# Performance work log

Hardware: AMD Instinct MI355X
Metric: run time of the kernel (lower is better)

## Reference

```python
import math
import jax, jax.numpy as jnp
import numpy as np

H = 4
C_HID = 32

def setup_inputs() -> dict:
    key = jax.random.key(0)
    ks = jax.random.split(key, 8)
    B, N, C = 1, 256, 128
    q_x = jax.random.normal(ks[0], (B, N, N, C), dtype=jnp.float32)
    kv_x = jax.random.normal(ks[1], (B, N, N, C), dtype=jnp.float32)
    tri_bias = jax.random.normal(ks[2], (B, 1, H, N, N), dtype=jnp.float32)
    mask_bias = jnp.zeros((B, N, 1, 1, N), dtype=jnp.float32)
    mask = jnp.ones((B, N, N, N), dtype=jnp.float32)
    s = 1.0 / math.sqrt(C)
    Wq = jax.random.normal(ks[3], (C, H * C_HID), dtype=jnp.float32) * s
    Wk = jax.random.normal(ks[4], (C, H * C_HID), dtype=jnp.float32) * s
    Wv = jax.random.normal(ks[5], (C, H * C_HID), dtype=jnp.float32) * s
    Wg = jax.random.normal(ks[6], (C, H * C_HID), dtype=jnp.float32) * s
    Wo = jax.random.normal(ks[7], (H * C_HID, C), dtype=jnp.float32) * s
    return {"q_x": q_x, "kv_x": kv_x, "tri_bias": tri_bias, "mask_bias": mask_bias,
            "mask": mask, "Wq": Wq, "Wk": Wk, "Wv": Wv, "Wg": Wg, "Wo": Wo}

def reference(q_x, kv_x, tri_bias, mask_bias, mask, Wq, Wk, Wv, Wg, Wo):
    # q_x/kv_x: [B, N, Q, C]; mask is unused in the non-kernel path (mask_bias carries it)
    lead = q_x.shape[:-1]  # [B, N, Q]
    def split_heads(t):  # [..., H*C_HID] -> [..., H, L, C_HID]
        t = t.reshape(t.shape[:-1] + (H, C_HID))
        return jnp.swapaxes(t, -2, -3)
    q = split_heads(q_x @ Wq) / math.sqrt(C_HID)   # [B, N, H, Q, C_hid]
    k = split_heads(kv_x @ Wk)                      # [B, N, H, K, C_hid]
    v = split_heads(kv_x @ Wv)                      # [B, N, H, K, C_hid]
    a = jnp.einsum('bnhqc,bnhkc->bnhqk', q, k)
    a = a + mask_bias + tri_bias                    # biases broadcast over [B, N, H, Q, K]
    a = jax.nn.softmax(a, axis=-1)
    o = jnp.einsum('bnhqk,bnhkc->bnhqc', a, v)      # [B, N, H, Q, C_hid]
    o = jnp.swapaxes(o, -2, -3)                     # [B, N, Q, H, C_hid]
    g = jax.nn.sigmoid(q_x @ Wg).reshape(lead + (H, C_HID))
    o = o * g
    o = o.reshape(lead + (H * C_HID,))
    return o @ Wo                                   # [B, N, Q, C]
```

## Files before the change

kernel.cpp:

```cpp
#include <hip/hip_runtime.h>
#include <hip/hip_bf16.h>

#define NDIM 256
#define QDIM 256
#define CDIM 128
#define HH 4
#define DD 32
#define RROWS (NDIM * QDIM)

__device__ __forceinline__ float bf2f(unsigned short u) {
    unsigned int x = ((unsigned int)u) << 16;
    return __uint_as_float(x);
}
__device__ __forceinline__ unsigned short f2bf(float f) {
    unsigned int x = __float_as_uint(f);
    unsigned int lsb = (x >> 16) & 1u;
    x += 0x7fffu + lsb;
    return (unsigned short)(x >> 16);
}

typedef __bf16 bf16x8v __attribute__((ext_vector_type(8)));
typedef float  f32x4v  __attribute__((ext_vector_type(4)));
union frag_u { uint4 u; bf16x8v v; };

__device__ __forceinline__ bf16x8v cvt8(float4 f0, float4 f1) {
    bf16x8v r;
    r[0] = (__bf16)f0.x; r[1] = (__bf16)f0.y; r[2] = (__bf16)f0.z; r[3] = (__bf16)f0.w;
    r[4] = (__bf16)f1.x; r[5] = (__bf16)f1.y; r[6] = (__bf16)f1.z; r[7] = (__bf16)f1.w;
    return r;
}

__global__ __launch_bounds__(256, 1) void prep_weights(
    const float* __restrict__ Wq, const float* __restrict__ Wk,
    const float* __restrict__ Wv, const float* __restrict__ Wg,
    const float* __restrict__ Wo, unsigned short* __restrict__ wt)
{
    __shared__ unsigned short t[16][130];
    const int p  = blockIdx.x >> 3;
    const int ch = blockIdx.x & 7;
    const float* __restrict__ W = (p == 0) ? Wq : (p == 1) ? Wk :
                                  (p == 2) ? Wv : (p == 3) ? Wg : Wo;
    const int tid = threadIdx.x;
    for (int idx = tid; idx < 2048; idx += 256) {
        int k = idx >> 7, n = idx & 127;
        t[k][n] = f2bf(W[(ch * 16 + k) * 128 + n]);
    }
    __syncthreads();
    unsigned short* dst = wt + (size_t)p * 16384;
    for (int idx = tid; idx < 2048; idx += 256) {
        int n = idx >> 4, k = idx & 15;
        dst[n * 128 + ch * 16 + k] = t[k][n];
    }
}

__global__ __launch_bounds__(512, 4) void proj_mfma(
    const float* __restrict__ qx, const float* __restrict__ kvx,
    const unsigned short* __restrict__ wt,
    unsigned short* __restrict__ q_ws, unsigned short* __restrict__ k_ws,
    unsigned short* __restrict__ v_ws, unsigned short* __restrict__ g_ws)
{
    __shared__ unsigned short wl[2 * 16384];
    const int tid = threadIdx.x;
    const int pp = blockIdx.y;
    const float* __restrict__ X = pp ? kvx : qx;
    const unsigned short* __restrict__ WtA = wt + (size_t)(pp ? 1 : 0) * 16384;
    const unsigned short* __restrict__ WtB = wt + (size_t)(pp ? 2 : 3) * 16384;

    const int wv   = tid >> 6;
    const int lane = tid & 63;
    const int col  = lane & 15;
    const int quad = lane >> 4;
    const int r0   = blockIdx.x * 128 + wv * 16;

    const float* __restrict__ arow = X + (size_t)(r0 + col) * 128 + quad * 8;
    float4 f[4][2];
#pragma unroll
    for (int kt = 0; kt < 4; ++kt) {
        f[kt][0] = *(const float4*)(arow + kt * 32);
        f[kt][1] = *(const float4*)(arow + kt * 32 + 4);
    }

#pragma unroll
    for (int i = 0; i < 8; ++i) {
        int v = i * 512 + tid;
        int mat = v >> 11;
        int r = (v >> 4) & 127;
        int s = v & 15;
        const unsigned short* src = (mat ? WtB : WtA) + r * 128 + s * 8;
        uint4 d = *(const uint4*)src;
        *(uint4*)&wl[mat * 16384 + r * 128 + ((s ^ (r & 7)) << 3)] = d;
    }
    __syncthreads();

    frag_u a[4];
#pragma unroll
    for (int kt = 0; kt < 4; ++kt) a[kt].v = cvt8(f[kt][0], f[kt][1]);

    f32x4v accA[8], accB[8];
#pragma unroll
    for (int nt = 0; nt < 8; ++nt) {
        accA[nt] = (f32x4v){0.f, 0.f, 0.f, 0.f};
        accB[nt] = (f32x4v){0.f, 0.f, 0.f, 0.f};
    }

    const int x7 = col & 7;
#pragma unroll
    for (int kt = 0; kt < 4; ++kt) {
#pragma unroll
        for (int nt = 0; nt < 8; ++nt) {
            int off = nt * 2048 + col * 128 + ((((kt << 2) | quad) ^ x7) << 3);
            frag_u b0, b1;
            b0.u = *(const uint4*)&wl[off];
            b1.u = *(const uint4*)&wl[16384 + off];
            accA[nt] = __builtin_amdgcn_mfma_f32_16x16x32_bf16(a[kt].v, b0.v, accA[nt], 0, 0, 0);
            accB[nt] = __builtin_amdgcn_mfma_f32_16x16x32_bf16(a[kt].v, b1.v, accB[nt], 0, 0, 0);
        }
    }

#pragma unroll
    for (int r = 0; r < 4; ++r) {
        int row = r0 + quad * 4 + r;
        int n = row >> 8;
        int si = row & 255;
#pragma unroll
        for (int nt = 0; nt < 8; ++nt) {
            int c = nt * 16 + col;
            int h = c >> 5, d = c & 31;
            size_t nh = (size_t)(n * HH + h);
            if (pp == 0) {
                float qv = accA[nt][r] * 0.17677669529663687f;
                q_ws[(nh * QDIM + si) * DD + d] = f2bf(qv);
                float s = 1.0f / (1.0f + __expf(-accB[nt][r]));
                g_ws[(nh * QDIM + si) * DD + d] = f2bf(s);
            } else {
                k_ws[(nh * QDIM + si) * DD + d] = f2bf(accA[nt][r]);
                v_ws[(nh * DD + d) * QDIM + si] = f2bf(accB[nt][r]);
            }
        }
    }
}

__global__ __launch_bounds__(256, 3) void attn_kernel(
    const unsigned short* __restrict__ q_ws, const unsigned short* __restrict__ k_ws,
    const unsigned short* __restrict__ v_ws, const unsigned short* __restrict__ g_ws,
    const float* __restrict__ tri, const float* __restrict__ mb,
    unsigned short* __restrict__ o_ws)
{
    __shared__ unsigned short vl[32 * 256];
    __shared__ unsigned short Pl[64 * 264];

    const int tid = threadIdx.x;
    const int b = blockIdx.x;
    const int L = (b & 7) * 512 + (b >> 3);
    const int qc = L & 3;
    const int n  = (L >> 2) & 255;
    const int h  = L >> 10;
    const size_t base  = (size_t)(n * HH + h) * QDIM * DD;
    const size_t vbase = (size_t)(n * HH + h) * DD * QDIM;

    const int wv   = tid >> 6;
    const int lane = tid & 63;
    const int col  = lane & 15;
    const int quad = lane >> 4;
    const int x7   = col & 7;
    const int qg   = qc * 64 + wv * 16 + col;

    frag_u vreg[4];
    const unsigned short* __restrict__ vsrc = v_ws + vbase;
#pragma unroll
    for (int j = 0; j < 4; ++j) {
        int idx = (wv * 4 + j) * 64 + lane;
        int d = idx >> 5, s = idx & 31;
        vreg[j].u = *(const uint4*)(vsrc + d * 256 + ((s ^ (d & 7)) << 3));
    }

    f32x4v bias[16];
#pragma unroll
    for (int mt = 0; mt < 16; ++mt) {
        int k0 = mt * 16 + quad * 4;
        float4 t4 = *(const float4*)&tri[((size_t)(h * 256 + qg)) * 256 + k0];
        float4 m4 = *(const float4*)&mb[n * 256 + k0];
        bias[mt][0] = t4.x + m4.x; bias[mt][1] = t4.y + m4.y;
        bias[mt][2] = t4.z + m4.z; bias[mt][3] = t4.w + m4.w;
    }

    frag_u bq;
    bq.u = *(const uint4*)(q_ws + base + (size_t)qg * DD + quad * 8);

    f32x4v acc[16];
#pragma unroll
    for (int mt = 0; mt < 16; ++mt) {
        frag_u ak;
        ak.u = *(const uint4*)(k_ws + base + (size_t)(mt * 16 + col) * DD + quad * 8);
        acc[mt] = __builtin_amdgcn_mfma_f32_16x16x32_bf16(ak.v, bq.v, bias[mt], 0, 0, 0);
    }

    float mx = -1e30f;
#pragma unroll
    for (int mt = 0; mt < 16; ++mt)
#pragma unroll
        for (int r = 0; r < 4; ++r) mx = fmaxf(mx, acc[mt][r]);
    mx = fmaxf(mx, __shfl_xor(mx, 16));
    mx = fmaxf(mx, __shfl_xor(mx, 32));

    float sum = 0.f;
#pragma unroll
    for (int mt = 0; mt < 16; ++mt)
#pragma unroll
        for (int r = 0; r < 4; ++r) {
            float e = __expf(acc[mt][r] - mx);
            acc[mt][r] = e;
            sum += e;
        }
    sum += __shfl_xor(sum, 16);
    sum += __shfl_xor(sum, 32);
    float inv = 1.0f / sum;

#pragma unroll
    for (int mt = 0; mt < 16; ++mt) {
        ushort4 pk;
        pk.x = f2bf(acc[mt][0]); pk.y = f2bf(acc[mt][1]);
        pk.z = f2bf(acc[mt][2]); pk.w = f2bf(acc[mt][3]);
        *(ushort4*)&Pl[(wv * 16 + col) * 264 + mt * 16 + quad * 4] = pk;
    }

#pragma unroll
    for (int j = 0; j < 4; ++j) {
        int idx = (wv * 4 + j) * 64 + lane;
        *(uint4*)&vl[idx << 3] = vreg[j].u;
    }
    __syncthreads();

    f32x4v o0 = {0.f, 0.f, 0.f, 0.f};
    f32x4v o1 = {0.f, 0.f, 0.f, 0.f};
#pragma unroll
    for (int kc = 0; kc < 8; ++kc) {
        int u0 = ((kc << 2) | quad) ^ x7;
        frag_u ap, b0, b1;
        ap.u = *(const uint4*)&Pl[(wv * 16 + col) * 264 + kc * 32 + quad * 8];
        b0.u = *(const uint4*)&vl[(col << 8) + (u0 << 3)];
        b1.u = *(const uint4*)&vl[((16 + col) << 8) + (u0 << 3)];
        o0 = __builtin_amdgcn_mfma_f32_16x16x32_bf16(ap.v, b0.v, o0, 0, 0, 0);
        o1 = __builtin_amdgcn_mfma_f32_16x16x32_bf16(ap.v, b1.v, o1, 0, 0, 0);
    }

#pragma unroll
    for (int r = 0; r < 4; ++r) {
        int qi = quad * 4 + r;
        int qglob = qc * 64 + wv * 16 + qi;
        float iv = __shfl(inv, qi);
        size_t ob = (((size_t)(n * HH + h)) * QDIM + qglob) * DD;
        float g0 = bf2f(g_ws[ob + col]);
        o_ws[ob + col] = f2bf(o0[r] * iv * g0);
        float g1 = bf2f(g_ws[ob + 16 + col]);
        o_ws[ob + 16 + col] = f2bf(o1[r] * iv * g1);
    }
}

__global__ __launch_bounds__(512, 4) void outproj_mfma(
    const unsigned short* __restrict__ o_ws, const unsigned short* __restrict__ wt,
    float* __restrict__ out)
{
    __shared__ unsigned short wl[16384];
    const int tid = threadIdx.x;
    const unsigned short* __restrict__ Wt = wt + 4 * 16384;

    const int wv   = tid >> 6;
    const int lane = tid & 63;
    const int col  = lane & 15;
    const int quad = lane >> 4;
    const int r0   = blockIdx.x * 128 + wv * 16;
    const int n    = r0 >> 8;
    const int q0   = r0 & 255;

    frag_u a[4];
#pragma unroll
    for (int kt = 0; kt < 4; ++kt)
        a[kt].u = *(const uint4*)(o_ws +
            ((size_t)(n * HH + kt) * QDIM + q0 + col) * DD + quad * 8);

#pragma unroll
    for (int i = 0; i < 4; ++i) {
        int v = i * 512 + tid;
        int r = v >> 4;
        int s = v & 15;
        uint4 d = *(const uint4*)(Wt + r * 128 + s * 8);
        *(uint4*)&wl[r * 128 + ((s ^ (r & 7)) << 3)] = d;
    }
    __syncthreads();

    f32x4v acc[8];
#pragma unroll
    for (int nt = 0; nt < 8; ++nt)
        acc[nt] = (f32x4v){0.f, 0.f, 0.f, 0.f};

    const int x7 = col & 7;
#pragma unroll
    for (int kt = 0; kt < 4; ++kt) {
#pragma unroll
        for (int nt = 0; nt < 8; ++nt) {
            int off = nt * 2048 + col * 128 + ((((kt << 2) | quad) ^ x7) << 3);
            frag_u b;
            b.u = *(const uint4*)&wl[off];
            acc[nt] = __builtin_amdgcn_mfma_f32_16x16x32_bf16(a[kt].v, b.v, acc[nt], 0, 0, 0);
        }
    }

#pragma unroll
    for (int r = 0; r < 4; ++r) {
        size_t row = r0 + quad * 4 + r;
#pragma unroll
        for (int nt = 0; nt < 8; ++nt)
            out[row * 128 + nt * 16 + col] = acc[nt][r];
    }
}

extern "C" void kernel_launch(void* const* d_in, const int* in_sizes, int n_in,
                              void* d_out, int out_size, void* d_ws, size_t ws_size,
                              hipStream_t stream) {
    const float* qx  = (const float*)d_in[0];
    const float* kvx = (const float*)d_in[1];
    const float* tri = (const float*)d_in[2];
    const float* mb  = (const float*)d_in[3];
    const float* Wq  = (const float*)d_in[5];
    const float* Wk  = (const float*)d_in[6];
    const float* Wv  = (const float*)d_in[7];
    const float* Wg  = (const float*)d_in[8];
    const float* Wo  = (const float*)d_in[9];
    float* out = (float*)d_out;

    unsigned short* ws = (unsigned short*)d_ws;
    const size_t RC = (size_t)RROWS * 128;
    unsigned short* q_ws = ws;
    unsigned short* k_ws = ws + RC;
    unsigned short* v_ws = ws + 2 * RC;
    unsigned short* g_ws = ws + 3 * RC;
    unsigned short* o_ws = ws + 4 * RC;
    unsigned short* wt   = ws + 5 * RC;

    prep_weights<<<dim3(40), 256, 0, stream>>>(Wq, Wk, Wv, Wg, Wo, wt);
    proj_mfma<<<dim3(RROWS / 128, 2), 512, 0, stream>>>(
        qx, kvx, wt, q_ws, k_ws, v_ws, g_ws);
    attn_kernel<<<dim3(4096), 256, 0, stream>>>(
        q_ws, k_ws, v_ws, g_ws, tri, mb, o_ws);
    outproj_mfma<<<dim3(RROWS / 128), 512, 0, stream>>>(o_ws, wt, out);
}
```

Baseline: 252.8 us.

## Keep weight fragments in registers and stage activation tiles in LDS for projections

The projection and output-projection GEMMs swap which operand goes through shared memory. Previously each block staged full 128x128 weight matrices in LDS (64KB or 32KB) and kept activation rows in registers. Now each wave holds a 16-column slice of the weights in registers, and a 64-row activation tile is converted to bf16 and staged in swizzled LDS (16KB). This cuts LDS footprint and per-block weight reload traffic, which should raise occupancy. The cost is twice as many blocks, and each wave now writes its outputs as one column slice, so stores to the q/k/g/out buffers may coalesce less well.

```diff
diff --git a/kernel.cpp b/kernel.cpp
--- a/kernel.cpp
+++ b/kernel.cpp
@@ -59,7 +59,7 @@
     unsigned short* __restrict__ q_ws, unsigned short* __restrict__ k_ws,
     unsigned short* __restrict__ v_ws, unsigned short* __restrict__ g_ws)
 {
-    __shared__ unsigned short wl[2 * 16384];
+    __shared__ unsigned short xl[64 * 128];
     const int tid = threadIdx.x;
     const int pp = blockIdx.y;
     const float* __restrict__ X = pp ? kvx : qx;
@@ -70,71 +70,69 @@
     const int lane = tid & 63;
     const int col  = lane & 15;
     const int quad = lane >> 4;
-    const int r0   = blockIdx.x * 128 + wv * 16;
-
-    const float* __restrict__ arow = X + (size_t)(r0 + col) * 128 + quad * 8;
-    float4 f[4][2];
+    const int r0   = blockIdx.x * 64;
+
+    frag_u bA[4], bB[4];
 #pragma unroll
     for (int kt = 0; kt < 4; ++kt) {
-        f[kt][0] = *(const float4*)(arow + kt * 32);
-        f[kt][1] = *(const float4*)(arow + kt * 32 + 4);
-    }
-
-#pragma unroll
-    for (int i = 0; i < 8; ++i) {
-        int v = i * 512 + tid;
-        int mat = v >> 11;
-        int r = (v >> 4) & 127;
-        int s = v & 15;
-        const unsigned short* src = (mat ? WtB : WtA) + r * 128 + s * 8;
-        uint4 d = *(const uint4*)src;
-        *(uint4*)&wl[mat * 16384 + r * 128 + ((s ^ (r & 7)) << 3)] = d;
+        size_t boff = (size_t)(wv * 16 + col) * 128 + kt * 32 + quad * 8;
+        bA[kt].u = *(const uint4*)(WtA + boff);
+        bB[kt].u = *(const uint4*)(WtB + boff);
+    }
+
+#pragma unroll
+    for (int i = 0; i < 2; ++i) {
+        int idx = i * 512 + tid;
+        int row = idx >> 4;
+        int s   = idx & 15;
+        const float* src = X + (size_t)(r0 + row) * 128 + s * 8;
+        float4 f0 = *(const float4*)src;
+        float4 f1 = *(const float4*)(src + 4);
+        frag_u t; t.v = cvt8(f0, f1);
+        *(uint4*)&xl[row * 128 + ((s ^ (row & 7)) << 3)] = t.u;
     }
     __syncthreads();
 
-    frag_u a[4];
-#pragma unroll
-    for (int kt = 0; kt < 4; ++kt) a[kt].v = cvt8(f[kt][0], f[kt][1]);
-
-    f32x4v accA[8], accB[8];
-#pragma unroll
-    for (int nt = 0; nt < 8; ++nt) {
-        accA[nt] = (f32x4v){0.f, 0.f, 0.f, 0.f};
-        accB[nt] = (f32x4v){0.f, 0.f, 0.f, 0.f};
+    f32x4v accA[4], accB[4];
+#pragma unroll
+    for (int mt = 0; mt < 4; ++mt) {
+        accA[mt] = (f32x4v){0.f, 0.f, 0.f, 0.f};
+        accB[mt] = (f32x4v){0.f, 0.f, 0.f, 0.f};
     }
 
     const int x7 = col & 7;
 #pragma unroll
-    for (int kt = 0; kt < 4; ++kt) {
-#pragma unroll
-        for (int nt = 0; nt < 8; ++nt) {
-            int off = nt * 2048 + col * 128 + ((((kt << 2) | quad) ^ x7) << 3);
-            frag_u b0, b1;
-            b0.u = *(const uint4*)&wl[off];
-            b1.u = *(const uint4*)&wl[16384 + off];
-            accA[nt] = __builtin_amdgcn_mfma_f32_16x16x32_bf16(a[kt].v, b0.v, accA[nt], 0, 0, 0);
-            accB[nt] = __builtin_amdgcn_mfma_f32_16x16x32_bf16(a[kt].v, b1.v, accB[nt], 0, 0, 0);
+    for (int mt = 0; mt < 4; ++mt) {
+        frag_u a[4];
+#pragma unroll
+        for (int kt = 0; kt < 4; ++kt)
+            a[kt].u = *(const uint4*)&xl[(mt * 16 + col) * 128 +
+                                         ((((kt << 2) | quad) ^ x7) << 3)];
+#pragma unroll
+        for (int kt = 0; kt < 4; ++kt) {
+            accA[mt] = __builtin_amdgcn_mfma_f32_16x16x32_bf16(a[kt].v, bA[kt].v, accA[mt], 0, 0, 0);
+            accB[mt] = __builtin_amdgcn_mfma_f32_16x16x32_bf16(a[kt].v, bB[kt].v, accB[mt], 0, 0, 0);
         }
     }
 
-#pragma unroll
-    for (int r = 0; r < 4; ++r) {
-        int row = r0 + quad * 4 + r;
-        int n = row >> 8;
-        int si = row & 255;
-#pragma unroll
-        for (int nt = 0; nt < 8; ++nt) {
-            int c = nt * 16 + col;
-            int h = c >> 5, d = c & 31;
+    const int c = wv * 16 + col;
+    const int h = c >> 5, d = c & 31;
+#pragma unroll
+    for (int mt = 0; mt < 4; ++mt) {
+#pragma unroll
+        for (int r = 0; r < 4; ++r) {
+            int row = r0 + mt * 16 + quad * 4 + r;
+            int n = row >> 8;
+            int si = row & 255;
             size_t nh = (size_t)(n * HH + h);
             if (pp == 0) {
-                float qv = accA[nt][r] * 0.17677669529663687f;
+                float qv = accA[mt][r] * 0.17677669529663687f;
                 q_ws[(nh * QDIM + si) * DD + d] = f2bf(qv);
-                float s = 1.0f / (1.0f + __expf(-accB[nt][r]));
+                float s = 1.0f / (1.0f + __expf(-accB[mt][r]));
                 g_ws[(nh * QDIM + si) * DD + d] = f2bf(s);
             } else {
-                k_ws[(nh * QDIM + si) * DD + d] = f2bf(accA[nt][r]);
-                v_ws[(nh * DD + d) * QDIM + si] = f2bf(accB[nt][r]);
+                k_ws[(nh * QDIM + si) * DD + d] = f2bf(accA[mt][r]);
+                v_ws[(nh * DD + d) * QDIM + si] = f2bf(accB[mt][r]);
             }
         }
     }
@@ -261,7 +259,7 @@
     const unsigned short* __restrict__ o_ws, const unsigned short* __restrict__ wt,
     float* __restrict__ out)
 {
-    __shared__ unsigned short wl[16384];
+    __shared__ unsigned short xl[64 * 128];
     const int tid = threadIdx.x;
     const unsigned short* __restrict__ Wt = wt + 4 * 16384;
 
@@ -269,50 +267,53 @@
     const int lane = tid & 63;
     const int col  = lane & 15;
     const int quad = lane >> 4;
-    const int r0   = blockIdx.x * 128 + wv * 16;
+    const int r0   = blockIdx.x * 64;
     const int n    = r0 >> 8;
     const int q0   = r0 & 255;
 
-    frag_u a[4];
+    frag_u bO[4];
 #pragma unroll
     for (int kt = 0; kt < 4; ++kt)
-        a[kt].u = *(const uint4*)(o_ws +
-            ((size_t)(n * HH + kt) * QDIM + q0 + col) * DD + quad * 8);
-
-#pragma unroll
-    for (int i = 0; i < 4; ++i) {
-        int v = i * 512 + tid;
-        int r = v >> 4;
-        int s = v & 15;
-        uint4 d = *(const uint4*)(Wt + r * 128 + s * 8);
-        *(uint4*)&wl[r * 128 + ((s ^ (r & 7)) << 3)] = d;
+        bO[kt].u = *(const uint4*)(Wt + (size_t)(wv * 16 + col) * 128 + kt * 32 + quad * 8);
+
+#pragma unroll
+    for (int i = 0; i < 2; ++i) {
+        int idx = i * 512 + tid;
+        int row = idx >> 4;
+        int s   = idx & 15;
+        int h   = s >> 2;
+        int d   = (s & 3) << 3;
+        uint4 v = *(const uint4*)(o_ws +
+            ((size_t)(n * HH + h) * QDIM + q0 + row) * DD + d);
+        *(uint4*)&xl[row * 128 + ((s ^ (row & 7)) << 3)] = v;
     }
     __syncthreads();
 
-    f32x4v acc[8];
-#pragma unroll
-    for (int nt = 0; nt < 8; ++nt)
-        acc[nt] = (f32x4v){0.f, 0.f, 0.f, 0.f};
+    f32x4v acc[4];
+#pragma unroll
+    for (int mt = 0; mt < 4; ++mt)
+        acc[mt] = (f32x4v){0.f, 0.f, 0.f, 0.f};
 
     const int x7 = col & 7;
 #pragma unroll
-    for (int kt = 0; kt < 4; ++kt) {
-#pragma unroll
-        for (int nt = 0; nt < 8; ++nt) {
-            int off = nt * 2048 + col * 128 + ((((kt << 2) | quad) ^ x7) << 3);
-            frag_u b;
-            b.u = *(const uint4*)&wl[off];
-            acc[nt] = __builtin_amdgcn_mfma_f32_16x16x32_bf16(a[kt].v, b.v, acc[nt], 0, 0, 0);
+    for (int mt = 0; mt < 4; ++mt) {
+        frag_u a[4];
+#pragma unroll
+        for (int kt = 0; kt < 4; ++kt)
+            a[kt].u = *(const uint4*)&xl[(mt * 16 + col) * 128 +
+                                         ((((kt << 2) | quad) ^ x7) << 3)];
+#pragma unroll
+        for (int kt = 0; kt < 4; ++kt)
+            acc[mt] = __builtin_amdgcn_mfma_f32_16x16x32_bf16(a[kt].v, bO[kt].v, acc[mt], 0, 0, 0);
+    }
+
+#pragma unroll
+    for (int mt = 0; mt < 4; ++mt)
+#pragma unroll
+        for (int r = 0; r < 4; ++r) {
+            size_t row = r0 + mt * 16 + quad * 4 + r;
+            out[row * 128 + wv * 16 + col] = acc[mt][r];
         }
-    }
-
-#pragma unroll
-    for (int r = 0; r < 4; ++r) {
-        size_t row = r0 + quad * 4 + r;
-#pragma unroll
-        for (int nt = 0; nt < 8; ++nt)
-            out[row * 128 + nt * 16 + col] = acc[nt][r];
-    }
 }
 
 extern "C" void kernel_launch(void* const* d_in, const int* in_sizes, int n_in,
@@ -339,9 +340,9 @@
     unsigned short* wt   = ws + 5 * RC;
 
     prep_weights<<<dim3(40), 256, 0, stream>>>(Wq, Wk, Wv, Wg, Wo, wt);
-    proj_mfma<<<dim3(RROWS / 128, 2), 512, 0, stream>>>(
+    proj_mfma<<<dim3(RROWS / 64, 2), 512, 0, stream>>>(
         qx, kvx, wt, q_ws, k_ws, v_ws, g_ws);
     attn_kernel<<<dim3(4096), 256, 0, stream>>>(
         q_ws, k_ws, v_ws, g_ws, tri, mb, o_ws);
-    outproj_mfma<<<dim3(RROWS / 128), 512, 0, stream>>>(o_ws, wt, out);
-}
+    outproj_mfma<<<dim3(RROWS / 64), 512, 0, stream>>>(o_ws, wt, out);
+}
```

Result: slower. 258.8 us (+2.4%).
